# Performance work log

Measured on AMD Instinct MI355X. Metric: run time of the kernel, lower is better.

Reference implementation:

```python
import jax, jax.numpy as jnp
import numpy as np

D_MODEL = 1280
NUM_HEADS = 16
GROUPS = 5
D_K = D_MODEL // NUM_HEADS  # 80
B, S = 4, 1024


def setup_inputs() -> dict:
    key = jax.random.key(0)
    ks = jax.random.split(key, 12)
    lim_dk = 1.0 / np.sqrt(D_K)
    lim_dm = 1.0 / np.sqrt(D_MODEL)
    return {
        "src": jax.random.normal(ks[0], (B, S, D_MODEL), jnp.float32),
        "k": jax.random.normal(ks[1], (B, S, D_MODEL), jnp.float32),
        "v": jax.random.normal(ks[2], (B, S, D_MODEL), jnp.float32),
        # per-head Linear(d_k, d_k) stacked: weight [H, d_k(out), d_k(in)], bias [H, d_k]
        "Wq": jax.random.uniform(ks[3], (NUM_HEADS, D_K, D_K), jnp.float32, -lim_dk, lim_dk),
        "bq": jax.random.uniform(ks[4], (NUM_HEADS, D_K), jnp.float32, -lim_dk, lim_dk),
        "Wk": jax.random.uniform(ks[5], (NUM_HEADS, D_K, D_K), jnp.float32, -lim_dk, lim_dk),
        "bk": jax.random.uniform(ks[6], (NUM_HEADS, D_K), jnp.float32, -lim_dk, lim_dk),
        "Wv": jax.random.uniform(ks[7], (NUM_HEADS, D_K, D_K), jnp.float32, -lim_dk, lim_dk),
        "bv": jax.random.uniform(ks[8], (NUM_HEADS, D_K), jnp.float32, -lim_dk, lim_dk),
        # output Linear(d_model, d_model)
        "Wo": jax.random.uniform(ks[9], (D_MODEL, D_MODEL), jnp.float32, -lim_dm, lim_dm),
        "bo": jax.random.uniform(ks[10], (D_MODEL,), jnp.float32, -lim_dm, lim_dm),
    }


def reference(src, k, v, Wq, bq, Wk, bk, Wv, bv, Wo, bo):
    # NOTE: original module ignores k, v args; q/k/v all derived from src.
    b, s, d = src.shape
    cpg = d // GROUPS
    # channel shuffle: [B,S,G,C] -> [B,S,C,G] -> [B,S,D]
    x = src.reshape(b, s, GROUPS, cpg).swapaxes(-1, -2).reshape(b, s, d)
    # split heads: [B, H, S, d_k]
    xh = x.reshape(b, s, NUM_HEADS, D_K).transpose(0, 2, 1, 3)
    # per-head distinct linears, batched over heads (torch Linear: x @ W.T + b)
    q = jnp.einsum("bhsd,hed->bhse", xh, Wq) + bq[None, :, None, :]
    kk = jnp.einsum("bhsd,hed->bhse", xh, Wk) + bk[None, :, None, :]
    vv = jnp.einsum("bhsd,hed->bhse", xh, Wv) + bv[None, :, None, :]
    scores = jnp.einsum("bhqd,bhkd->bhqk", q, kk) / jnp.sqrt(jnp.float32(D_K))
    p = jax.nn.softmax(scores, axis=-1)
    heads = jnp.einsum("bhqk,bhkd->bhqd", p, vv)
    concat = heads.transpose(0, 2, 1, 3).reshape(b, s, d)
    return concat @ Wo.T + bo
```

## Files before the change

### kernel.cpp

```cpp
#include <hip/hip_runtime.h>
#include <hip/hip_bf16.h>

#define D_MODEL 1280
#define NUM_HEADS 16
#define D_K 80
#define DP 96
#define SEQ 1024
#define BATCH 4
#define BH (BATCH*NUM_HEADS)

typedef __hip_bfloat16 bf16;
typedef short short8 __attribute__((ext_vector_type(8)));
typedef short short4v __attribute__((ext_vector_type(4)));
typedef float f32x4 __attribute__((ext_vector_type(4)));

__device__ __forceinline__ float b2f(bf16 x) { return __bfloat162float(x); }
__device__ __forceinline__ bf16 f2b(float x) { return __float2bfloat16(x); }
__device__ __forceinline__ short bbits(float x) {
    union { bf16 b; short s; } u; u.b = __float2bfloat16(x); return u.s;
}

#define MFMA16(a, b, c) __builtin_amdgcn_mfma_f32_16x16x32_bf16(a, b, c, 0, 0, 0)

__global__ __launch_bounds__(256) void cvt_all_kernel(
    const float* __restrict__ Wq, const float* __restrict__ Wk,
    const float* __restrict__ Wv, bf16* __restrict__ Wcat,
    const float* __restrict__ Wo, bf16* __restrict__ Wb)
{
    if (blockIdx.x < 1440) {
        int idx = blockIdx.x * 256 + threadIdx.x;
        int col = idx % 96;
        int row = (idx / 96) % 240;
        int h   = idx / (96 * 240);
        int mat = row / 80, e = row % 80;
        const float* W = (mat == 0) ? Wq : (mat == 1) ? Wk : Wv;
        float v = (col < 80) ? W[(size_t)(h * 80 + e) * 80 + col] : 0.f;
        Wcat[idx] = f2b(v);
    } else {
        int idx = ((blockIdx.x - 1440) * 256 + threadIdx.x) * 4;
        float4 v = *(const float4*)(Wo + idx);
        Wb[idx]     = f2b(v.x);
        Wb[idx + 1] = f2b(v.y);
        Wb[idx + 2] = f2b(v.z);
        Wb[idx + 3] = f2b(v.w);
    }
}

__global__ __launch_bounds__(256) void qkv_kernel(
    const float* __restrict__ src,
    const float* __restrict__ bq, const float* __restrict__ bk,
    const float* __restrict__ bv, const bf16* __restrict__ Wcat,
    bf16* __restrict__ Qb, bf16* __restrict__ Kb, bf16* __restrict__ Vg)
{
    __shared__ bf16 Xs[128 * 104];
    const int h = blockIdx.y;
    const int b = blockIdx.x >> 3;
    const int s0 = (blockIdx.x & 7) * 128;
    const int tid = threadIdx.x;
    const int wave = tid >> 6, lane = tid & 63;
    const int lquad = lane >> 4, lcol = lane & 15;
    const int bh = b * NUM_HEADS + h;

    #pragma unroll
    for (int it = 0; it < 10; it++) {
        int idx = tid + it * 256;
        int i = idx / 20, rem = idx % 20, c = rem >> 2, q4 = rem & 3;
        float4 v = *(const float4*)(src + (size_t)(b * SEQ + s0 + i) * D_MODEL
                                    + c * 256 + h * 16 + q4 * 4);
        bf16* x = Xs + i * 104 + c;
        x[(q4 * 4 + 0) * 5] = f2b(v.x);
        x[(q4 * 4 + 1) * 5] = f2b(v.y);
        x[(q4 * 4 + 2) * 5] = f2b(v.z);
        x[(q4 * 4 + 3) * 5] = f2b(v.w);
    }
    {
        int i = tid >> 1, half = tid & 1;
        *(uint4*)(Xs + i * 104 + 80 + half * 8) = make_uint4(0, 0, 0, 0);
    }
    __syncthreads();

    short8 xf[2][3];
    #pragma unroll
    for (int mt = 0; mt < 2; mt++)
        #pragma unroll
        for (int ks = 0; ks < 3; ks++)
            xf[mt][ks] = *(const short8*)(Xs + (wave*32 + mt*16 + lcol)*104 + ks*32 + lquad*8);

    const bf16* Wh = Wcat + (size_t)h * 240 * 96;
    const float qscale = 1.4426950408889634f * 0.11180339887498949f;

    #pragma unroll
    for (int mat = 0; mat < 2; mat++) {
        const bf16* Wm = Wh + mat * 80 * 96;
        short8 wf[5][3];
        #pragma unroll
        for (int n = 0; n < 5; n++)
            #pragma unroll
            for (int ks = 0; ks < 3; ks++)
                wf[n][ks] = *(const short8*)(Wm + (n*16 + lcol)*96 + ks*32 + lquad*8);

        f32x4 acc[2][5];
        #pragma unroll
        for (int mt = 0; mt < 2; mt++)
            #pragma unroll
            for (int n = 0; n < 5; n++)
                #pragma unroll
                for (int r = 0; r < 4; r++) acc[mt][n][r] = 0.f;

        #pragma unroll
        for (int ks = 0; ks < 3; ks++)
            #pragma unroll
            for (int n = 0; n < 5; n++) {
                acc[0][n] = MFMA16(xf[0][ks], wf[n][ks], acc[0][n]);
                acc[1][n] = MFMA16(xf[1][ks], wf[n][ks], acc[1][n]);
            }

        const float* bias = (mat == 0) ? bq : bk;
        bf16* Out = (mat == 0) ? Qb : Kb;
        const float scale = (mat == 0) ? qscale : 1.f;
        #pragma unroll
        for (int n = 0; n < 5; n++) {
            float bb = bias[h * 80 + n * 16 + lcol];
            #pragma unroll
            for (int mt = 0; mt < 2; mt++)
                #pragma unroll
                for (int r = 0; r < 4; r++) {
                    int srow = s0 + wave*32 + mt*16 + lquad*4 + r;
                    Out[((size_t)bh * SEQ + srow) * DP + n*16 + lcol] =
                        f2b((acc[mt][n][r] + bb) * scale);
                }
        }
    }
    {
        int i = tid >> 1, half = tid & 1;
        size_t row = ((size_t)bh * SEQ + s0 + i) * DP + 80 + half * 8;
        *(uint4*)(Qb + row) = make_uint4(0, 0, 0, 0);
        *(uint4*)(Kb + row) = make_uint4(0, 0, 0, 0);
    }

    {
        const bf16* Wm = Wh + 2 * 80 * 96;
        short8 wf[5][3];
        #pragma unroll
        for (int m = 0; m < 5; m++)
            #pragma unroll
            for (int ks = 0; ks < 3; ks++)
                wf[m][ks] = *(const short8*)(Wm + (m*16 + lcol)*96 + ks*32 + lquad*8);

        f32x4 acc[5][2];
        #pragma unroll
        for (int m = 0; m < 5; m++)
            #pragma unroll
            for (int nt = 0; nt < 2; nt++)
                #pragma unroll
                for (int r = 0; r < 4; r++) acc[m][nt][r] = 0.f;

        #pragma unroll
        for (int ks = 0; ks < 3; ks++)
            #pragma unroll
            for (int m = 0; m < 5; m++) {
                acc[m][0] = MFMA16(wf[m][ks], xf[0][ks], acc[m][0]);
                acc[m][1] = MFMA16(wf[m][ks], xf[1][ks], acc[m][1]);
            }

        #pragma unroll
        for (int m = 0; m < 5; m++) {
            float4 bb4 = *(const float4*)(bv + h * 80 + m * 16 + lquad * 4);
            float bb[4] = {bb4.x, bb4.y, bb4.z, bb4.w};
            #pragma unroll
            for (int nt = 0; nt < 2; nt++)
                #pragma unroll
                for (int r = 0; r < 4; r++) {
                    int e = m*16 + lquad*4 + r;
                    int token = s0 + wave*32 + nt*16 + lcol;
                    Vg[((size_t)bh * D_K + e) * SEQ + token] =
                        f2b(acc[m][nt][r] + bb[r]);
                }
        }
    }
}

__global__ __launch_bounds__(128, 2) void attn_kernel(
    const bf16* __restrict__ Qb, const bf16* __restrict__ Kb,
    const bf16* __restrict__ Vg, bf16* __restrict__ Cc)
{
    __shared__ char smem[38144];
    bf16* Qs = (bf16*)smem;
    bf16* Ks = (bf16*)(smem + 13312);
    bf16* Vt = (bf16*)(smem + 26624);

    const int tid = threadIdx.x;
    const int wave = tid >> 6, lane = tid & 63;
    const int lquad = lane >> 4, lcol = lane & 15;
    const int bh = blockIdx.x;
    const int b = bh >> 4, h = bh & 15;
    const int q0 = blockIdx.y * 64;

    const uint4* Kg  = (const uint4*)(Kb + (size_t)bh * SEQ * DP);
    const bf16*  Vgb = Vg + (size_t)bh * D_K * SEQ;

    const int i0 = tid, i1 = tid + 128, i2 = tid + 256,
              i3 = tid + 384, i4 = tid + 512, i5 = tid + 640;
    const int kd0 = (i0/12)*104 + (i0%12)*8, kd1 = (i1/12)*104 + (i1%12)*8,
              kd2 = (i2/12)*104 + (i2%12)*8, kd3 = (i3/12)*104 + (i3%12)*8,
              kd4 = (i4/12)*104 + (i4%12)*8, kd5 = (i5/12)*104 + (i5%12)*8;
    const int vd0 = (i0>>3)*72 + (i0&7)*8, vd1 = (i1>>3)*72 + (i1&7)*8,
              vd2 = (i2>>3)*72 + (i2&7)*8, vd3 = (i3>>3)*72 + (i3&7)*8,
              vd4 = (i4>>3)*72 + (i4&7)*8;
    const int vg0 = (i0>>3)*SEQ + (i0&7)*8, vg1 = (i1>>3)*SEQ + (i1&7)*8,
              vg2 = (i2>>3)*SEQ + (i2&7)*8, vg3 = (i3>>3)*SEQ + (i3&7)*8,
              vg4 = (i4>>3)*SEQ + (i4&7)*8;

    {
        const uint4* qg = (const uint4*)(Qb + ((size_t)bh * SEQ + q0) * DP);
        #pragma unroll
        for (int i = 0; i < 6; i++) {
            int idx = tid + i * 128, r = idx / 12, c = idx % 12;
            *(uint4*)(Qs + r * 104 + c * 8) = qg[idx];
        }
    }
    __syncthreads();

    short8 qf[2][3];
    #pragma unroll
    for (int nt = 0; nt < 2; nt++)
        #pragma unroll
        for (int ks = 0; ks < 3; ks++)
            qf[nt][ks] = *(const short8*)(Qs + (wave*32 + nt*16 + lcol)*104 + ks*32 + lquad*8);

    *(uint4*)(Ks + kd0) = Kg[i0];
    *(uint4*)(Ks + kd1) = Kg[i1];
    *(uint4*)(Ks + kd2) = Kg[i2];
    *(uint4*)(Ks + kd3) = Kg[i3];
    *(uint4*)(Ks + kd4) = Kg[i4];
    *(uint4*)(Ks + kd5) = Kg[i5];
    *(uint4*)(Vt + vd0) = *(const uint4*)(Vgb + vg0);
    *(uint4*)(Vt + vd1) = *(const uint4*)(Vgb + vg1);
    *(uint4*)(Vt + vd2) = *(const uint4*)(Vgb + vg2);
    *(uint4*)(Vt + vd3) = *(const uint4*)(Vgb + vg3);
    *(uint4*)(Vt + vd4) = *(const uint4*)(Vgb + vg4);
    __syncthreads();

    f32x4 Oacc[2][5];
    #pragma unroll
    for (int mt = 0; mt < 2; mt++)
        #pragma unroll
        for (int ne = 0; ne < 5; ne++)
            #pragma unroll
            for (int r = 0; r < 4; r++) Oacc[mt][ne][r] = 0.f;

    f32x4 lsum4[2];
    #pragma unroll
    for (int nt = 0; nt < 2; nt++)
        #pragma unroll
        for (int r = 0; r < 4; r++) lsum4[nt][r] = 0.f;

    bf16* Pw = (bf16*)(smem + wave * 4608);
    const f32x4 fzero = {0.f, 0.f, 0.f, 0.f};

    for (int kt = 0; kt < 16; kt++) {
        const int ktn = (kt + 1) & 15;
        uint4 kA = Kg[ktn * 768 + i0];
        uint4 kB = Kg[ktn * 768 + i1];
        uint4 kC = Kg[ktn * 768 + i2];
        uint4 kD = Kg[ktn * 768 + i3];
        uint4 kE = Kg[ktn * 768 + i4];
        uint4 kF = Kg[ktn * 768 + i5];
        uint4 vA = *(const uint4*)(Vgb + vg0 + ktn * 64);
        uint4 vB = *(const uint4*)(Vgb + vg1 + ktn * 64);
        uint4 vC = *(const uint4*)(Vgb + vg2 + ktn * 64);
        uint4 vD = *(const uint4*)(Vgb + vg3 + ktn * 64);
        uint4 vE = *(const uint4*)(Vgb + vg4 + ktn * 64);

        f32x4 st[4][2];
        __builtin_amdgcn_s_setprio(1);
        #pragma unroll
        for (int mt = 0; mt < 4; mt++) {
            short8 af = *(const short8*)(Ks + (mt*16 + lcol)*104 + lquad*8);
            st[mt][0] = MFMA16(af, qf[0][0], fzero);
            st[mt][1] = MFMA16(af, qf[1][0], fzero);
        }
        #pragma unroll
        for (int ks = 1; ks < 3; ks++)
            #pragma unroll
            for (int mt = 0; mt < 4; mt++) {
                short8 af = *(const short8*)(Ks + (mt*16 + lcol)*104 + ks*32 + lquad*8);
                st[mt][0] = MFMA16(af, qf[0][ks], st[mt][0]);
                st[mt][1] = MFMA16(af, qf[1][ks], st[mt][1]);
            }
        __builtin_amdgcn_s_setprio(0);

        #pragma unroll
        for (int nt = 0; nt < 2; nt++)
            #pragma unroll
            for (int mt = 0; mt < 4; mt++) {
                short4v pk;
                #pragma unroll
                for (int r = 0; r < 4; r++) {
                    float p = __builtin_amdgcn_exp2f(st[mt][nt][r]);
                    lsum4[nt][r] += p;
                    pk[r] = bbits(p);
                }
                *(short4v*)(Pw + (nt*16 + lcol)*72 + mt*16 + lquad*4) = pk;
            }

        __builtin_amdgcn_s_setprio(1);
        #pragma unroll
        for (int js = 0; js < 2; js++) {
            short8 pf0 = *(const short8*)(Pw + lcol*72 + js*32 + lquad*8);
            short8 pf1 = *(const short8*)(Pw + (16 + lcol)*72 + js*32 + lquad*8);
            #pragma unroll
            for (int ne = 0; ne < 5; ne++) {
                short8 vfx = *(const short8*)(Vt + (ne*16 + lcol)*72 + js*32 + lquad*8);
                Oacc[0][ne] = MFMA16(pf0, vfx, Oacc[0][ne]);
                Oacc[1][ne] = MFMA16(pf1, vfx, Oacc[1][ne]);
            }
        }
        __builtin_amdgcn_s_setprio(0);

        __syncthreads();
        *(uint4*)(Ks + kd0) = kA;
        *(uint4*)(Ks + kd1) = kB;
        *(uint4*)(Ks + kd2) = kC;
        *(uint4*)(Ks + kd3) = kD;
        *(uint4*)(Ks + kd4) = kE;
        *(uint4*)(Ks + kd5) = kF;
        *(uint4*)(Vt + vd0) = vA;
        *(uint4*)(Vt + vd1) = vB;
        *(uint4*)(Vt + vd2) = vC;
        *(uint4*)(Vt + vd3) = vD;
        *(uint4*)(Vt + vd4) = vE;
        __syncthreads();
    }

    float inv[2];
    #pragma unroll
    for (int nt = 0; nt < 2; nt++) {
        float s = (lsum4[nt][0] + lsum4[nt][1]) + (lsum4[nt][2] + lsum4[nt][3]);
        s += __shfl_xor(s, 16);
        s += __shfl_xor(s, 32);
        inv[nt] = 1.f / s;
    }
    #pragma unroll
    for (int mt = 0; mt < 2; mt++) {
        f32x4 li;
        #pragma unroll
        for (int r = 0; r < 4; r++)
            li[r] = __shfl(inv[mt], (lane & 48) | (lquad*4 + r));
        #pragma unroll
        for (int ne = 0; ne < 5; ne++)
            #pragma unroll
            for (int r = 0; r < 4; r++) {
                int s_row = q0 + wave*32 + mt*16 + lquad*4 + r;
                int e = ne*16 + lcol;
                Cc[(size_t)(b * SEQ + s_row) * D_MODEL + h * D_K + e] =
                    f2b(Oacc[mt][ne][r] * li[r]);
            }
    }
}

__global__ __launch_bounds__(256) void proj_kernel(
    const bf16* __restrict__ Cc, const bf16* __restrict__ Wb,
    const float* __restrict__ bo, float* __restrict__ out)
{
    __shared__ bf16 As[128 * 72];
    __shared__ bf16 Bs[128 * 72];
    const int tid = threadIdx.x;
    const int wave = tid >> 6, lane = tid & 63;
    const int lquad = lane >> 4, lcol = lane & 15;
    const int t0 = blockIdx.x * 128, o0 = blockIdx.y * 128;
    const int mrow = (wave & 1) * 64, ncol = (wave >> 1) * 64;

    f32x4 acc[4][4];
    #pragma unroll
    for (int mt = 0; mt < 4; mt++)
        #pragma unroll
        for (int nt = 0; nt < 4; nt++)
            #pragma unroll
            for (int r = 0; r < 4; r++) acc[mt][nt][r] = 0.f;

    for (int kc = 0; kc < 20; kc++) {
        __syncthreads();
        #pragma unroll
        for (int i = 0; i < 4; i++) {
            int idx = tid + i * 256;
            int r = idx >> 3, c = idx & 7;
            *(uint4*)(As + r * 72 + c * 8) =
                *(const uint4*)(Cc + (size_t)(t0 + r) * D_MODEL + kc * 64 + c * 8);
            *(uint4*)(Bs + r * 72 + c * 8) =
                *(const uint4*)(Wb + (size_t)(o0 + r) * D_MODEL + kc * 64 + c * 8);
        }
        __syncthreads();
        #pragma unroll
        for (int ks = 0; ks < 2; ks++) {
            short8 am[4], bn[4];
            #pragma unroll
            for (int t = 0; t < 4; t++) {
                am[t] = *(const short8*)(As + (mrow + t*16 + lcol)*72 + ks*32 + lquad*8);
                bn[t] = *(const short8*)(Bs + (ncol + t*16 + lcol)*72 + ks*32 + lquad*8);
            }
            #pragma unroll
            for (int mt = 0; mt < 4; mt++)
                #pragma unroll
                for (int nt = 0; nt < 4; nt++)
                    acc[mt][nt] = MFMA16(am[mt], bn[nt], acc[mt][nt]);
        }
    }

    #pragma unroll
    for (int nt = 0; nt < 4; nt++) {
        float bias = bo[o0 + ncol + nt*16 + lcol];
        #pragma unroll
        for (int mt = 0; mt < 4; mt++)
            #pragma unroll
            for (int r = 0; r < 4; r++)
                out[(size_t)(t0 + mrow + mt*16 + lquad*4 + r) * D_MODEL
                    + o0 + ncol + nt*16 + lcol] = acc[mt][nt][r] + bias;
    }
}

extern "C" void kernel_launch(void* const* d_in, const int* in_sizes, int n_in,
                              void* d_out, int out_size, void* d_ws, size_t ws_size,
                              hipStream_t stream) {
    const float* src = (const float*)d_in[0];
    const float* Wq = (const float*)d_in[3];
    const float* bq = (const float*)d_in[4];
    const float* Wk = (const float*)d_in[5];
    const float* bk = (const float*)d_in[6];
    const float* Wv = (const float*)d_in[7];
    const float* bv = (const float*)d_in[8];
    const float* Wo = (const float*)d_in[9];
    const float* bo = (const float*)d_in[10];
    float* out = (float*)d_out;

    char* ws = (char*)d_ws;
    bf16* Qb = (bf16*)(ws);
    bf16* Kb = (bf16*)(ws + (size_t)12582912);
    bf16* Vg = (bf16*)(ws + (size_t)25165824);
    bf16* Cc = (bf16*)(ws + (size_t)35651584);
    bf16* Wcat = (bf16*)(ws + (size_t)35651584);
    bf16* Wb = (bf16*)(ws + (size_t)46137344);

    cvt_all_kernel<<<dim3(3040), 256, 0, stream>>>(Wq, Wk, Wv, Wcat, Wo, Wb);
    qkv_kernel<<<dim3(BATCH * SEQ / 128, NUM_HEADS), 256, 0, stream>>>(
        src, bq, bk, bv, Wcat, Qb, Kb, Vg);
    attn_kernel<<<dim3(BH, SEQ / 64), 128, 0, stream>>>(Qb, Kb, Vg, Cc);
    proj_kernel<<<dim3(SEQ * BATCH / 128, D_MODEL / 128), 256, 0, stream>>>(
        Cc, Wb, bo, out);
}
```

Baseline: 191.6 us.

## Prefetch proj tiles into registers and load QKV inputs directly without LDS shuffle

```diff
diff --git a/kernel.cpp b/kernel.cpp
--- a/kernel.cpp
+++ b/kernel.cpp
@@ -33,8 +33,9 @@
         int row = (idx / 96) % 240;
         int h   = idx / (96 * 240);
         int mat = row / 80, e = row % 80;
+        int c = col >> 4, j = col & 15;
         const float* W = (mat == 0) ? Wq : (mat == 1) ? Wk : Wv;
-        float v = (col < 80) ? W[(size_t)(h * 80 + e) * 80 + col] : 0.f;
+        float v = (col < 80) ? W[(size_t)(h * 80 + e) * 80 + (j * 5 + c)] : 0.f;
         Wcat[idx] = f2b(v);
     } else {
         int idx = ((blockIdx.x - 1440) * 256 + threadIdx.x) * 4;
@@ -52,7 +53,6 @@
     const float* __restrict__ bv, const bf16* __restrict__ Wcat,
     bf16* __restrict__ Qb, bf16* __restrict__ Kb, bf16* __restrict__ Vg)
 {
-    __shared__ bf16 Xs[128 * 104];
     const int h = blockIdx.y;
     const int b = blockIdx.x >> 3;
     const int s0 = (blockIdx.x & 7) * 128;
@@ -61,33 +61,31 @@
     const int lquad = lane >> 4, lcol = lane & 15;
     const int bh = b * NUM_HEADS + h;
 
-    #pragma unroll
-    for (int it = 0; it < 10; it++) {
-        int idx = tid + it * 256;
-        int i = idx / 20, rem = idx % 20, c = rem >> 2, q4 = rem & 3;
-        float4 v = *(const float4*)(src + (size_t)(b * SEQ + s0 + i) * D_MODEL
-                                    + c * 256 + h * 16 + q4 * 4);
-        bf16* x = Xs + i * 104 + c;
-        x[(q4 * 4 + 0) * 5] = f2b(v.x);
-        x[(q4 * 4 + 1) * 5] = f2b(v.y);
-        x[(q4 * 4 + 2) * 5] = f2b(v.z);
-        x[(q4 * 4 + 3) * 5] = f2b(v.w);
-    }
-    {
-        int i = tid >> 1, half = tid & 1;
-        *(uint4*)(Xs + i * 104 + 80 + half * 8) = make_uint4(0, 0, 0, 0);
-    }
-    __syncthreads();
-
     short8 xf[2][3];
     #pragma unroll
     for (int mt = 0; mt < 2; mt++)
         #pragma unroll
-        for (int ks = 0; ks < 3; ks++)
-            xf[mt][ks] = *(const short8*)(Xs + (wave*32 + mt*16 + lcol)*104 + ks*32 + lquad*8);
+        for (int ks = 0; ks < 3; ks++) {
+            const int c  = 2 * ks + (lquad >> 1);
+            const int j0 = (lquad & 1) * 8;
+            short8 t = {0, 0, 0, 0, 0, 0, 0, 0};
+            if (c < 5) {
+                const float* p = src
+                    + (size_t)(b * SEQ + s0 + wave * 32 + mt * 16 + lcol) * D_MODEL
+                    + c * 256 + h * 16 + j0;
+                float4 v0 = *(const float4*)p;
+                float4 v1 = *(const float4*)(p + 4);
+                t[0] = bbits(v0.x); t[1] = bbits(v0.y);
+                t[2] = bbits(v0.z); t[3] = bbits(v0.w);
+                t[4] = bbits(v1.x); t[5] = bbits(v1.y);
+                t[6] = bbits(v1.z); t[7] = bbits(v1.w);
+            }
+            xf[mt][ks] = t;
+        }
 
     const bf16* Wh = Wcat + (size_t)h * 240 * 96;
     const float qscale = 1.4426950408889634f * 0.11180339887498949f;
+    const f32x4 fzero = {0.f, 0.f, 0.f, 0.f};
 
     #pragma unroll
     for (int mat = 0; mat < 2; mat++) {
@@ -101,14 +99,12 @@
 
         f32x4 acc[2][5];
         #pragma unroll
-        for (int mt = 0; mt < 2; mt++)
-            #pragma unroll
-            for (int n = 0; n < 5; n++)
-                #pragma unroll
-                for (int r = 0; r < 4; r++) acc[mt][n][r] = 0.f;
-
-        #pragma unroll
-        for (int ks = 0; ks < 3; ks++)
+        for (int n = 0; n < 5; n++) {
+            acc[0][n] = MFMA16(xf[0][0], wf[n][0], fzero);
+            acc[1][n] = MFMA16(xf[1][0], wf[n][0], fzero);
+        }
+        #pragma unroll
+        for (int ks = 1; ks < 3; ks++)
             #pragma unroll
             for (int n = 0; n < 5; n++) {
                 acc[0][n] = MFMA16(xf[0][ks], wf[n][ks], acc[0][n]);
@@ -149,14 +145,12 @@
 
         f32x4 acc[5][2];
         #pragma unroll
-        for (int m = 0; m < 5; m++)
-            #pragma unroll
-            for (int nt = 0; nt < 2; nt++)
-                #pragma unroll
-                for (int r = 0; r < 4; r++) acc[m][nt][r] = 0.f;
-
-        #pragma unroll
-        for (int ks = 0; ks < 3; ks++)
+        for (int m = 0; m < 5; m++) {
+            acc[m][0] = MFMA16(wf[m][0], xf[0][0], fzero);
+            acc[m][1] = MFMA16(wf[m][0], xf[1][0], fzero);
+        }
+        #pragma unroll
+        for (int ks = 1; ks < 3; ks++)
             #pragma unroll
             for (int m = 0; m < 5; m++) {
                 acc[m][0] = MFMA16(wf[m][ks], xf[0][ks], acc[m][0]);
@@ -371,6 +365,28 @@
     const int t0 = blockIdx.x * 128, o0 = blockIdx.y * 128;
     const int mrow = (wave & 1) * 64, ncol = (wave >> 1) * 64;
 
+    const int i0 = tid, i1 = tid + 256, i2 = tid + 512, i3 = tid + 768;
+    const int d0 = (i0>>3)*72 + (i0&7)*8, d1 = (i1>>3)*72 + (i1&7)*8,
+              d2 = (i2>>3)*72 + (i2&7)*8, d3 = (i3>>3)*72 + (i3&7)*8;
+    const size_t gA0 = (size_t)(t0 + (i0>>3))*D_MODEL + (i0&7)*8;
+    const size_t gA1 = (size_t)(t0 + (i1>>3))*D_MODEL + (i1&7)*8;
+    const size_t gA2 = (size_t)(t0 + (i2>>3))*D_MODEL + (i2&7)*8;
+    const size_t gA3 = (size_t)(t0 + (i3>>3))*D_MODEL + (i3&7)*8;
+    const size_t gB0 = (size_t)(o0 + (i0>>3))*D_MODEL + (i0&7)*8;
+    const size_t gB1 = (size_t)(o0 + (i1>>3))*D_MODEL + (i1&7)*8;
+    const size_t gB2 = (size_t)(o0 + (i2>>3))*D_MODEL + (i2&7)*8;
+    const size_t gB3 = (size_t)(o0 + (i3>>3))*D_MODEL + (i3&7)*8;
+
+    *(uint4*)(As + d0) = *(const uint4*)(Cc + gA0);
+    *(uint4*)(As + d1) = *(const uint4*)(Cc + gA1);
+    *(uint4*)(As + d2) = *(const uint4*)(Cc + gA2);
+    *(uint4*)(As + d3) = *(const uint4*)(Cc + gA3);
+    *(uint4*)(Bs + d0) = *(const uint4*)(Wb + gB0);
+    *(uint4*)(Bs + d1) = *(const uint4*)(Wb + gB1);
+    *(uint4*)(Bs + d2) = *(const uint4*)(Wb + gB2);
+    *(uint4*)(Bs + d3) = *(const uint4*)(Wb + gB3);
+    __syncthreads();
+
     f32x4 acc[4][4];
     #pragma unroll
     for (int mt = 0; mt < 4; mt++)
@@ -380,17 +396,17 @@
             for (int r = 0; r < 4; r++) acc[mt][nt][r] = 0.f;
 
     for (int kc = 0; kc < 20; kc++) {
-        __syncthreads();
-        #pragma unroll
-        for (int i = 0; i < 4; i++) {
-            int idx = tid + i * 256;
-            int r = idx >> 3, c = idx & 7;
-            *(uint4*)(As + r * 72 + c * 8) =
-                *(const uint4*)(Cc + (size_t)(t0 + r) * D_MODEL + kc * 64 + c * 8);
-            *(uint4*)(Bs + r * 72 + c * 8) =
-                *(const uint4*)(Wb + (size_t)(o0 + r) * D_MODEL + kc * 64 + c * 8);
-        }
-        __syncthreads();
+        const int kn = (kc < 19) ? (kc + 1) * 64 : 0;
+        uint4 pa0 = *(const uint4*)(Cc + gA0 + kn);
+        uint4 pa1 = *(const uint4*)(Cc + gA1 + kn);
+        uint4 pa2 = *(const uint4*)(Cc + gA2 + kn);
+        uint4 pa3 = *(const uint4*)(Cc + gA3 + kn);
+        uint4 pb0 = *(const uint4*)(Wb + gB0 + kn);
+        uint4 pb1 = *(const uint4*)(Wb + gB1 + kn);
+        uint4 pb2 = *(const uint4*)(Wb + gB2 + kn);
+        uint4 pb3 = *(const uint4*)(Wb + gB3 + kn);
+
+        __builtin_amdgcn_s_setprio(1);
         #pragma unroll
         for (int ks = 0; ks < 2; ks++) {
             short8 am[4], bn[4];
@@ -405,6 +421,18 @@
                 for (int nt = 0; nt < 4; nt++)
                     acc[mt][nt] = MFMA16(am[mt], bn[nt], acc[mt][nt]);
         }
+        __builtin_amdgcn_s_setprio(0);
+
+        __syncthreads();
+        *(uint4*)(As + d0) = pa0;
+        *(uint4*)(As + d1) = pa1;
+        *(uint4*)(As + d2) = pa2;
+        *(uint4*)(As + d3) = pa3;
+        *(uint4*)(Bs + d0) = pb0;
+        *(uint4*)(Bs + d1) = pb1;
+        *(uint4*)(Bs + d2) = pb2;
+        *(uint4*)(Bs + d3) = pb3;
+        __syncthreads();
     }
 
     #pragma unroll
```

Measured after the change: 192.1 us. No clear change (+0.3%).
